# Kernel tuning notes

Hardware: AMD Instinct MI355X
Metric: run time of the kernel (lower is better)

Reference implementation:

```python
import jax, jax.numpy as jnp
import numpy as np

N = 8192
IN_CH = 256
OUT_CH = 64
LEAKY_ALPHA = 0.5
NEG_INF = -9e15  # -9000000000000000.0 from the source


def setup_inputs() -> dict:
    key = jax.random.key(0)
    k1, k2, k3, k4 = jax.random.split(key, 4)
    h = jax.random.normal(k1, (N, IN_CH), dtype=jnp.float32)
    adj = jax.random.randint(k2, (N, N), 0, 2, dtype=jnp.int32)
    # Xavier-uniform-style init for parameters
    limW = float(np.sqrt(6.0 / (IN_CH + OUT_CH)))
    W = jax.random.uniform(k3, (IN_CH, OUT_CH), dtype=jnp.float32, minval=-limW, maxval=limW)
    lima = float(np.sqrt(6.0 / (2 * OUT_CH + 1)))
    a = jax.random.uniform(k4, (2 * OUT_CH, 1), dtype=jnp.float32, minval=-lima, maxval=lima)
    return {"h": h, "adj": adj, "W": W, "a": a}


def reference(h, adj, W, a):
    # Wh: [N, out]
    Wh = h @ W
    # additive attention score: e[i,j] = leakyrelu(Wh[i]@a1 + Wh[j]@a2)
    Wh1 = Wh @ a[:OUT_CH]   # [N, 1]
    Wh2 = Wh @ a[OUT_CH:]   # [N, 1]
    e = Wh1 + Wh2.T         # [N, N]
    e = jnp.where(e >= 0, e, LEAKY_ALPHA * e)  # LeakyReLU(0.5)
    # adjacency masking + row softmax
    att = jnp.where(adj > 0, e, jnp.float32(NEG_INF))
    att = jax.nn.softmax(att, axis=1)
    # dropout is identity in eval mode (training=False)
    h_prime = att @ Wh      # [N, out]
    # concat=True branch applies ReLU on the output
    return jax.nn.relu(h_prime)
```

## Files before the change

kernel.cpp:

```cpp
#include <hip/hip_runtime.h>
#include <stdint.h>

#define NN 8192
#define INC 256
#define OUTC 64
#define LOG2E 1.4426950408889634f
#define JSPLIT 4

typedef __bf16 bf16x8 __attribute__((ext_vector_type(8)));
typedef float f32x4 __attribute__((ext_vector_type(4)));

__device__ __forceinline__ unsigned short f2bf(float x) {
    union { float f; unsigned u; } v; v.f = x;
    unsigned u = v.u;
    u += 0x7fffu + ((u >> 16) & 1u);
    return (unsigned short)(u >> 16);
}

#if __has_builtin(__builtin_amdgcn_exp2f)
#define EXP2(x) __builtin_amdgcn_exp2f(x)
#else
#define EXP2(x) exp2f(x)
#endif

__global__ __launch_bounds__(256) void gat_k1(
        const float* __restrict__ h, const float* __restrict__ W,
        const float* __restrict__ a,
        unsigned short* __restrict__ WhTf, float* __restrict__ Wh1,
        float* __restrict__ Wh2) {
    __shared__ float Ws[256 * 65];
    __shared__ float hs[16 * INC];
    __shared__ float Wa1s[256], Wa2s[256], as_[128];
    __shared__ unsigned short wt[OUTC][16];
    const int r0 = blockIdx.x * 16;
    const int t  = threadIdx.x;
    if (t < 128) as_[t] = a[t];
    #pragma unroll
    for (int it = 0; it < 16; ++it) {
        int idx = it * 1024 + t * 4;
        float4 v = *reinterpret_cast<const float4*>(W + idx);
        int k = idx >> 6, c = idx & 63;
        float* dst = &Ws[k * 65 + c];
        dst[0] = v.x; dst[1] = v.y; dst[2] = v.z; dst[3] = v.w;
    }
    #pragma unroll
    for (int it = 0; it < 4; ++it) {
        int idx = it * 1024 + t * 4;
        float4 v = *reinterpret_cast<const float4*>(h + (size_t)r0 * INC + idx);
        hs[idx] = v.x; hs[idx + 1] = v.y; hs[idx + 2] = v.z; hs[idx + 3] = v.w;
    }
    __syncthreads();
    {
        float s1 = 0.f, s2 = 0.f;
        #pragma unroll 8
        for (int c = 0; c < OUTC; ++c) {
            float w = Ws[t * 65 + c];
            s1 = fmaf(w, as_[c], s1);
            s2 = fmaf(w, as_[OUTC + c], s2);
        }
        Wa1s[t] = s1; Wa2s[t] = s2;
    }
    __syncthreads();
    const int w = t >> 6, lane = t & 63;
    const int c = lane;
    const float* hr = &hs[w * 4 * INC];
    float acc0 = 0.f, acc1 = 0.f, acc2 = 0.f, acc3 = 0.f;
    #pragma unroll 8
    for (int k = 0; k < INC; ++k) {
        float wv = Ws[k * 65 + c];
        acc0 = fmaf(hr[k],           wv, acc0);
        acc1 = fmaf(hr[INC + k],     wv, acc1);
        acc2 = fmaf(hr[2 * INC + k], wv, acc2);
        acc3 = fmaf(hr[3 * INC + k], wv, acc3);
    }
    float s1r[4] = {0.f, 0.f, 0.f, 0.f}, s2r[4] = {0.f, 0.f, 0.f, 0.f};
    #pragma unroll
    for (int kk = 0; kk < 4; ++kk) {
        int k = kk * 64 + lane;
        float wa1v = Wa1s[k], wa2v = Wa2s[k];
        #pragma unroll
        for (int r = 0; r < 4; ++r) {
            float hv = hr[r * INC + k];
            s1r[r] = fmaf(hv, wa1v, s1r[r]);
            s2r[r] = fmaf(hv, wa2v, s2r[r]);
        }
    }
    #pragma unroll
    for (int r = 0; r < 4; ++r) {
        float s1 = s1r[r], s2 = s2r[r];
        #pragma unroll
        for (int off = 32; off; off >>= 1) {
            s1 += __shfl_xor(s1, off, 64);
            s2 += __shfl_xor(s2, off, 64);
        }
        if (lane == 0) { Wh1[r0 + w * 4 + r] = s1; Wh2[r0 + w * 4 + r] = s2; }
    }
    wt[c][w * 4 + 0] = f2bf(acc0);
    wt[c][w * 4 + 1] = f2bf(acc1);
    wt[c][w * 4 + 2] = f2bf(acc2);
    wt[c][w * 4 + 3] = f2bf(acc3);
    __syncthreads();
    if (t < 128) {
        int m = t & 15, ct = (t >> 4) & 3, oct = t >> 6;
        int Kb = r0 >> 5;
        int qh = (r0 >> 3) & 3;
        int lanef = (qh + oct) * 16 + m;
        int cidx = ct * 16 + m;
        ushort4 v0, v1;
        v0.x = wt[cidx][oct * 8 + 0]; v0.y = wt[cidx][oct * 8 + 1];
        v0.z = wt[cidx][oct * 8 + 2]; v0.w = wt[cidx][oct * 8 + 3];
        v1.x = wt[cidx][oct * 8 + 4]; v1.y = wt[cidx][oct * 8 + 5];
        v1.z = wt[cidx][oct * 8 + 6]; v1.w = wt[cidx][oct * 8 + 7];
        unsigned short* dst = WhTf + (((size_t)(Kb * 4 + ct)) << 9) + lanef * 8;
        *reinterpret_cast<ushort4*>(dst)     = v0;
        *reinterpret_cast<ushort4*>(dst + 4) = v1;
    }
}

__global__ void gat_k2(const float* __restrict__ Wh2, float* __restrict__ M) {
    __shared__ float red[16];
    int t = threadIdx.x;
    float4 v0 = *reinterpret_cast<const float4*>(Wh2 + t * 4);
    float4 v1 = *reinterpret_cast<const float4*>(Wh2 + 4096 + t * 4);
    float m = fmaxf(fmaxf(fmaxf(v0.x, v0.y), fmaxf(v0.z, v0.w)),
                    fmaxf(fmaxf(v1.x, v1.y), fmaxf(v1.z, v1.w)));
    #pragma unroll
    for (int off = 32; off; off >>= 1) m = fmaxf(m, __shfl_xor(m, off, 64));
    if ((t & 63) == 0) red[t >> 6] = m;
    __syncthreads();
    if (t == 0) {
        float mm = red[0];
        #pragma unroll
        for (int i = 1; i < 16; ++i) mm = fmaxf(mm, red[i]);
        *M = mm;
    }
}

__global__ __launch_bounds__(256, 8) void gat_k3(
        const int* __restrict__ adj, const unsigned short* __restrict__ WhTf,
        const float* __restrict__ Wh1, const float* __restrict__ Wh2,
        const float* __restrict__ Mp, float* __restrict__ pacc,
        float* __restrict__ pl) {
    __shared__ float accs[4][16 * OUTC];
    __shared__ float ls[4][16];
    const int r0 = blockIdx.x * 16;
    const int split = blockIdx.y;
    const int jbase = split * 64;
    const int t = threadIdx.x;
    const int w = t >> 6, lane = t & 63;
    const int m = lane & 15, q = lane >> 4;
    const int qo = q * 8;
    const int row = r0 + m;
    const float wh1 = Wh1[row];
    const float Mv = *Mp;
    const float sM = wh1 + Mv;
    const float mhat = fmaxf(sM, 0.5f * sM);
    const float mh2 = mhat * LOG2E;
    const int* __restrict__ arow = adj + (size_t)row * NN;
    f32x4 acc[4] = {{0,0,0,0},{0,0,0,0},{0,0,0,0},{0,0,0,0}};
    float lpart = 0.f;

    const int jt0 = jbase + w;
    int4 c0 = *reinterpret_cast<const int4*>(arow + (size_t)jt0 * 32 + qo);
    int4 c1 = *reinterpret_cast<const int4*>(arow + (size_t)jt0 * 32 + qo + 4);
    int4 d0 = *reinterpret_cast<const int4*>(arow + (size_t)(jt0 + 4) * 32 + qo);
    int4 d1 = *reinterpret_cast<const int4*>(arow + (size_t)(jt0 + 4) * 32 + qo + 4);

    #pragma unroll 2
    for (int i = 0; i < 16; ++i) {
        const int jt = jt0 + i * 4;
        const unsigned short* fb = WhTf + (size_t)jt * 2048 + lane * 8;
        bf16x8 bv0 = *reinterpret_cast<const bf16x8*>(fb);
        bf16x8 bv1 = *reinterpret_cast<const bf16x8*>(fb + 512);
        bf16x8 bv2 = *reinterpret_cast<const bf16x8*>(fb + 1024);
        bf16x8 bv3 = *reinterpret_cast<const bf16x8*>(fb + 1536);
        const int jb = jt * 32 + qo;
        float4 s0 = *reinterpret_cast<const float4*>(Wh2 + jb);
        float4 s1 = *reinterpret_cast<const float4*>(Wh2 + jb + 4);
        const int jn = (i < 14) ? (jt + 8) : jt0;
        const int* __restrict__ an = arow + (size_t)jn * 32 + qo;
        int4 e0 = *reinterpret_cast<const int4*>(an);
        int4 e1 = *reinterpret_cast<const int4*>(an + 4);
        float sv[8] = {s0.x, s0.y, s0.z, s0.w, s1.x, s1.y, s1.z, s1.w};
        int   av[8] = {c0.x, c0.y, c0.z, c0.w, c1.x, c1.y, c1.z, c1.w};
        float p[8];
        #pragma unroll
        for (int e = 0; e < 8; ++e) {
            float s  = wh1 + sv[e];
            float lk = fmaxf(s, 0.5f * s);
            float ar = fmaf(lk, LOG2E, -mh2);
            float pe = EXP2(ar);
            p[e] = (av[e] > 0) ? pe : 0.f;
        }
        lpart += ((p[0] + p[1]) + (p[2] + p[3])) + ((p[4] + p[5]) + (p[6] + p[7]));
        bf16x8 af;
        #pragma unroll
        for (int e = 0; e < 8; ++e) af[e] = (__bf16)p[e];
        acc[0] = __builtin_amdgcn_mfma_f32_16x16x32_bf16(af, bv0, acc[0], 0, 0, 0);
        acc[1] = __builtin_amdgcn_mfma_f32_16x16x32_bf16(af, bv1, acc[1], 0, 0, 0);
        acc[2] = __builtin_amdgcn_mfma_f32_16x16x32_bf16(af, bv2, acc[2], 0, 0, 0);
        acc[3] = __builtin_amdgcn_mfma_f32_16x16x32_bf16(af, bv3, acc[3], 0, 0, 0);
        c0 = d0; c1 = d1; d0 = e0; d1 = e1;
    }
    #pragma unroll
    for (int ct = 0; ct < 4; ++ct)
        #pragma unroll
        for (int r = 0; r < 4; ++r)
            accs[w][(q * 4 + r) * OUTC + ct * 16 + m] = acc[ct][r];
    float l = lpart;
    l += __shfl_xor(l, 16, 64);
    l += __shfl_xor(l, 32, 64);
    if (lane < 16) ls[w][lane] = l;
    __syncthreads();
    float* pa = pacc + ((size_t)split * NN + r0) * OUTC;
    #pragma unroll
    for (int e = t; e < 16 * OUTC; e += 256) {
        int rr = e >> 6, cc = e & 63;
        float s = (accs[0][e] + accs[1][e]) + (accs[2][e] + accs[3][e]);
        pa[e] = s;
        if (cc == 0) pl[(size_t)split * NN + r0 + rr] =
            (ls[0][rr] + ls[1][rr]) + (ls[2][rr] + ls[3][rr]);
    }
}

__global__ __launch_bounds__(256) void gat_k4(
        const float* __restrict__ pacc, const float* __restrict__ pl,
        float* __restrict__ out) {
    const int idx4 = (blockIdx.x * 256 + threadIdx.x) * 4;
    const int row = idx4 >> 6;
    f32x4 s = {0.f, 0.f, 0.f, 0.f};
    float l = 0.f;
    #pragma unroll
    for (int sp = 0; sp < JSPLIT; ++sp) {
        f32x4 v = *reinterpret_cast<const f32x4*>(pacc + (size_t)sp * NN * OUTC + idx4);
        s += v;
        l += pl[(size_t)sp * NN + row];
    }
    float rl = 1.0f / l;
    f32x4 o;
    #pragma unroll
    for (int e = 0; e < 4; ++e) {
        float v = s[e] * rl;
        o[e] = v > 0.f ? v : 0.f;
    }
    *reinterpret_cast<f32x4*>(out + idx4) = o;
}

extern "C" void kernel_launch(void* const* d_in, const int* in_sizes, int n_in,
                              void* d_out, int out_size, void* d_ws, size_t ws_size,
                              hipStream_t stream) {
    const float* h   = (const float*)d_in[0];
    const int*   adj = (const int*)d_in[1];
    const float* W   = (const float*)d_in[2];
    const float* a   = (const float*)d_in[3];
    float* out = (float*)d_out;

    char* base = (char*)d_ws;
    float* Wh1 = (float*)(base);
    float* Wh2 = (float*)(base + 32768);
    float* Mp  = (float*)(base + 65536);
    unsigned short* WhTf = (unsigned short*)(base + 69632);
    float* pacc = (float*)(base + 2166784);
    float* pl   = (float*)(base + 2166784 + (size_t)JSPLIT * NN * OUTC * 4);

    gat_k1<<<NN / 16, 256, 0, stream>>>(h, W, a, WhTf, Wh1, Wh2);
    gat_k2<<<1, 1024, 0, stream>>>(Wh2, Mp);
    gat_k3<<<dim3(NN / 16, JSPLIT), 256, 0, stream>>>(adj, WhTf, Wh1, Wh2, Mp, pacc, pl);
    gat_k4<<<NN * OUTC / 1024, 256, 0, stream>>>(pacc, pl, out);
}
```

Baseline: 426.4 us.

## Pack adjacency into transposed bitmask in a pre-pass before attention kernel

Adds a pre-pass kernel that reads the int32 adjacency matrix once and packs each 32-column chunk into a 32-bit mask, stored transposed so the attention kernel reads one coalesced word per row per tile. The attention kernel drops its register-prefetched int4 adjacency loads and tests mask bits instead, and its occupancy hint drops from 8 to 6. The full 256 MB adjacency read still happens, now in a separate kernel, plus an extra 8 MB mask write and read. The attention kernel's traffic shrinks a lot, but total bytes do not fall and the prefetch overlap is lost.

```diff
diff --git a/kernel.cpp b/kernel.cpp
--- a/kernel.cpp
+++ b/kernel.cpp
@@ -22,6 +22,23 @@
 #else
 #define EXP2(x) exp2f(x)
 #endif
+
+__global__ __launch_bounds__(256) void gat_pack(
+        const int* __restrict__ adj, uint32_t* __restrict__ maskT) {
+    const int row = blockIdx.x;
+    const int tx  = threadIdx.x;
+    const int* p = adj + (size_t)row * NN + tx * 32;
+    uint32_t m = 0;
+    #pragma unroll
+    for (int k = 0; k < 8; ++k) {
+        int4 v = *reinterpret_cast<const int4*>(p + k * 4);
+        m |= (uint32_t)v.x << (k * 4 + 0);
+        m |= (uint32_t)v.y << (k * 4 + 1);
+        m |= (uint32_t)v.z << (k * 4 + 2);
+        m |= (uint32_t)v.w << (k * 4 + 3);
+    }
+    maskT[(size_t)tx * NN + row] = m;
+}
 
 __global__ __launch_bounds__(256) void gat_k1(
         const float* __restrict__ h, const float* __restrict__ W,
@@ -136,8 +153,8 @@
     }
 }
 
-__global__ __launch_bounds__(256, 8) void gat_k3(
-        const int* __restrict__ adj, const unsigned short* __restrict__ WhTf,
+__global__ __launch_bounds__(256, 6) void gat_k3(
+        const uint32_t* __restrict__ maskT, const unsigned short* __restrict__ WhTf,
         const float* __restrict__ Wh1, const float* __restrict__ Wh2,
         const float* __restrict__ Mp, float* __restrict__ pacc,
         float* __restrict__ pl) {
@@ -145,7 +162,6 @@
     __shared__ float ls[4][16];
     const int r0 = blockIdx.x * 16;
     const int split = blockIdx.y;
-    const int jbase = split * 64;
     const int t = threadIdx.x;
     const int w = t >> 6, lane = t & 63;
     const int m = lane & 15, q = lane >> 4;
@@ -156,19 +172,14 @@
     const float sM = wh1 + Mv;
     const float mhat = fmaxf(sM, 0.5f * sM);
     const float mh2 = mhat * LOG2E;
-    const int* __restrict__ arow = adj + (size_t)row * NN;
     f32x4 acc[4] = {{0,0,0,0},{0,0,0,0},{0,0,0,0},{0,0,0,0}};
     float lpart = 0.f;
-
-    const int jt0 = jbase + w;
-    int4 c0 = *reinterpret_cast<const int4*>(arow + (size_t)jt0 * 32 + qo);
-    int4 c1 = *reinterpret_cast<const int4*>(arow + (size_t)jt0 * 32 + qo + 4);
-    int4 d0 = *reinterpret_cast<const int4*>(arow + (size_t)(jt0 + 4) * 32 + qo);
-    int4 d1 = *reinterpret_cast<const int4*>(arow + (size_t)(jt0 + 4) * 32 + qo + 4);
+    const int jt0 = split * 64 + w;
 
     #pragma unroll 2
     for (int i = 0; i < 16; ++i) {
         const int jt = jt0 + i * 4;
+        uint32_t mk = maskT[(size_t)jt * NN + row];
         const unsigned short* fb = WhTf + (size_t)jt * 2048 + lane * 8;
         bf16x8 bv0 = *reinterpret_cast<const bf16x8*>(fb);
         bf16x8 bv1 = *reinterpret_cast<const bf16x8*>(fb + 512);
@@ -177,12 +188,8 @@
         const int jb = jt * 32 + qo;
         float4 s0 = *reinterpret_cast<const float4*>(Wh2 + jb);
         float4 s1 = *reinterpret_cast<const float4*>(Wh2 + jb + 4);
-        const int jn = (i < 14) ? (jt + 8) : jt0;
-        const int* __restrict__ an = arow + (size_t)jn * 32 + qo;
-        int4 e0 = *reinterpret_cast<const int4*>(an);
-        int4 e1 = *reinterpret_cast<const int4*>(an + 4);
         float sv[8] = {s0.x, s0.y, s0.z, s0.w, s1.x, s1.y, s1.z, s1.w};
-        int   av[8] = {c0.x, c0.y, c0.z, c0.w, c1.x, c1.y, c1.z, c1.w};
+        const uint32_t mq = mk >> qo;
         float p[8];
         #pragma unroll
         for (int e = 0; e < 8; ++e) {
@@ -190,7 +197,7 @@
             float lk = fmaxf(s, 0.5f * s);
             float ar = fmaf(lk, LOG2E, -mh2);
             float pe = EXP2(ar);
-            p[e] = (av[e] > 0) ? pe : 0.f;
+            p[e] = ((mq >> e) & 1u) ? pe : 0.f;
         }
         lpart += ((p[0] + p[1]) + (p[2] + p[3])) + ((p[4] + p[5]) + (p[6] + p[7]));
         bf16x8 af;
@@ -200,7 +207,6 @@
         acc[1] = __builtin_amdgcn_mfma_f32_16x16x32_bf16(af, bv1, acc[1], 0, 0, 0);
         acc[2] = __builtin_amdgcn_mfma_f32_16x16x32_bf16(af, bv2, acc[2], 0, 0, 0);
         acc[3] = __builtin_amdgcn_mfma_f32_16x16x32_bf16(af, bv3, acc[3], 0, 0, 0);
-        c0 = d0; c1 = d1; d0 = e0; d1 = e1;
     }
     #pragma unroll
     for (int ct = 0; ct < 4; ++ct)
@@ -262,9 +268,11 @@
     unsigned short* WhTf = (unsigned short*)(base + 69632);
     float* pacc = (float*)(base + 2166784);
     float* pl   = (float*)(base + 2166784 + (size_t)JSPLIT * NN * OUTC * 4);
-
+    uint32_t* maskT = (uint32_t*)(base + 10686464);
+
+    gat_pack<<<NN, 256, 0, stream>>>(adj, maskT);
     gat_k1<<<NN / 16, 256, 0, stream>>>(h, W, a, WhTf, Wh1, Wh2);
     gat_k2<<<1, 1024, 0, stream>>>(Wh2, Mp);
-    gat_k3<<<dim3(NN / 16, JSPLIT), 256, 0, stream>>>(adj, WhTf, Wh1, Wh2, Mp, pacc, pl);
+    gat_k3<<<dim3(NN / 16, JSPLIT), 256, 0, stream>>>(maskT, WhTf, Wh1, Wh2, Mp, pacc, pl);
     gat_k4<<<NN * OUTC / 1024, 256, 0, stream>>>(pacc, pl, out);
 }
```

Measured after the change: 422.6 us. About the same (-0.9%).
